# Performance work log

Measured on AMD Instinct MI355X. Metric: run time of the kernel, lower is better.

Reference implementation:

```python
import jax, jax.numpy as jnp
import numpy as np

B, T, H = 2, 2048, 1024
NH_R, HD_R = 4, 256            # RWKV6 heads / head_dim
EXP, HD_M = 2, 64
DI = EXP * H                   # mamba inner = 2048
NH_M = DI // HD_M              # 32 mamba heads
DS = 128                       # mamba d_state
CK = 4                         # causal conv kernel
FFN = 4 * H
EPS = 1e-6


def rms(x, w, eps=EPS):
    return w * x * jax.lax.rsqrt(jnp.mean(x * x, -1, keepdims=True) + eps)


def setup_inputs() -> dict:
    key = jax.random.key(0)
    ks = iter(jax.random.split(key, 32))
    def w(shape, scale=0.02):
        return jax.random.normal(next(ks), shape, jnp.float32) * scale
    return dict(
        x=w((B, T, H), 1.0),
        ln_w=jnp.ones((H,), jnp.float32),
        r_w=w((H, H)), k_w=w((H, H)), v_w=w((H, H)), g_w=w((H, H)), dw_w=w((H, H)),
        u=w((NH_R, HD_R), 0.5),
        gn_w=jnp.ones((H,), jnp.float32),
        o_w=w((H, H)),
        in_proj=w((H, 2 * DI + 2 * DS + NH_M)),
        conv_w=w((DI + 2 * DS, CK), 0.1),
        conv_b=jnp.zeros((DI + 2 * DS,), jnp.float32),
        dt_bias=w((NH_M,), 0.1),
        A_log=jnp.log(jnp.arange(1, NH_M + 1, dtype=jnp.float32)),
        D_m=w((NH_M,), 0.5),
        m_norm_w=jnp.ones((DI,), jnp.float32),
        out_proj=w((DI, H)),
        gate_w=jnp.zeros((2 * H, 1), jnp.float32),   # zero-init per module
        gate_b=jnp.zeros((1,), jnp.float32),         # logit(0.5) = 0
        ffn_ln_w=jnp.ones((H,), jnp.float32),
        ffn_w1=w((H, FFN)),
        ffn_w2=w((FFN, H)),
    )


def _rwkv6(nx, r_w, k_w, v_w, g_w, dw_w, u, gn_w, o_w):
    r = (nx @ r_w).reshape(B, T, NH_R, HD_R)
    k = (nx @ k_w).reshape(B, T, NH_R, HD_R)
    v = (nx @ v_w).reshape(B, T, NH_R, HD_R)
    g = jax.nn.silu(nx @ g_w)                                  # output gate
    wdec = jnp.exp(-jnp.exp(nx @ dw_w)).reshape(B, T, NH_R, HD_R)  # data-dep decay in (0,1)
    tm = lambda a: a.transpose(1, 0, 2, 3)                     # [T,B,h,d]

    def step(S, inp):  # S: [B,h,K,V]
        rt, kt, vt, wt = inp
        kv = kt[..., :, None] * vt[..., None, :]
        o = jnp.einsum('bhk,bhkv->bhv', rt, S + u[..., :, None] * kv)
        return wt[..., :, None] * S + kv, o

    S0 = jnp.zeros((B, NH_R, HD_R, HD_R), nx.dtype)
    _, o = jax.lax.scan(step, S0, (tm(r), tm(k), tm(v), tm(wdec)))
    o = o.transpose(1, 0, 2, 3)                                # [B,T,h,d]
    o = o * jax.lax.rsqrt(jnp.mean(o * o, -1, keepdims=True) + EPS)  # per-head RMS (group norm)
    o = o.reshape(B, T, H) * gn_w
    return (o * g) @ o_w


def _mamba2(nx, in_proj, conv_w, conv_b, dt_bias, A_log, D_m, m_norm_w, out_proj):
    zxbcdt = nx @ in_proj
    z, xBC, dt = jnp.split(zxbcdt, [DI, 2 * DI + 2 * DS], axis=-1)
    xp = jnp.pad(xBC, ((0, 0), (CK - 1, 0), (0, 0)))           # causal depthwise conv
    xBC = sum(xp[:, i:i + T, :] * conv_w[:, i] for i in range(CK)) + conv_b
    xBC = jax.nn.silu(xBC)
    xm, Bm, Cm = jnp.split(xBC, [DI, DI + DS], axis=-1)
    xm = xm.reshape(B, T, NH_M, HD_M)
    dt = jax.nn.softplus(dt + dt_bias)                          # [B,T,nh]
    A = -jnp.exp(A_log)                                         # [nh]

    def step(h, inp):  # h: [B,nh,hd,ds]
        xt, Bt, Ct, dtt = inp
        h = h * jnp.exp(dtt * A)[..., None, None] + (dtt[..., None] * xt)[..., None] * Bt[:, None, None, :]
        y = jnp.einsum('bhds,bs->bhd', h, Ct)
        return h, y

    h0 = jnp.zeros((B, NH_M, HD_M, DS), nx.dtype)
    _, y = jax.lax.scan(step, h0, (xm.transpose(1, 0, 2, 3), Bm.transpose(1, 0, 2), Cm.transpose(1, 0, 2), dt.transpose(1, 0, 2)))
    y = y.transpose(1, 0, 2, 3) + D_m[None, None, :, None] * xm
    y = y.reshape(B, T, DI)
    y = rms(y * jax.nn.silu(z), m_norm_w)                       # gated RMSNorm
    return y @ out_proj


def reference(x, ln_w, r_w, k_w, v_w, g_w, dw_w, u, gn_w, o_w,
              in_proj, conv_w, conv_b, dt_bias, A_log, D_m, m_norm_w, out_proj,
              gate_w, gate_b, ffn_ln_w, ffn_w1, ffn_w2):
    nx = rms(x, ln_w)
    o_r = _rwkv6(nx, r_w, k_w, v_w, g_w, dw_w, u, gn_w, o_w)
    o_m = _mamba2(nx, in_proj, conv_w, conv_b, dt_bias, A_log, D_m, m_norm_w, out_proj)
    gate = jax.nn.sigmoid(jnp.concatenate([o_r, o_m], -1) @ gate_w + gate_b)  # [B,T,1]
    x = x + gate * o_r + (1.0 - gate) * o_m
    x = x + jax.nn.gelu(rms(x, ffn_ln_w) @ ffn_w1, approximate=False) @ ffn_w2
    return x
```

## Files before the change

### kernel.cpp

```cpp
#include <hip/hip_runtime.h>
#include <hip/hip_bf16.h>
#include <stdint.h>

#define B_ 2
#define T_ 2048
#define H_ 1024
#define M_ 4096
#define DI 2048
#define DS 128
#define CONVD 2304
#define LD2 4480
#define EPS_ 1e-6f

typedef __bf16 bf16x8 __attribute__((ext_vector_type(8)));
typedef float f32x4 __attribute__((ext_vector_type(4)));
typedef uint32_t u32x4 __attribute__((ext_vector_type(4)));

__device__ __forceinline__ unsigned short f2bfu(float f) {
    union { float f; uint32_t u; } a; a.f = f;
    uint32_t r = a.u + 0x7FFFu + ((a.u >> 16) & 1u);
    return (unsigned short)(r >> 16);
}
__device__ __forceinline__ float bfu2f(unsigned short u) {
    union { uint32_t u; float f; } a; a.u = ((uint32_t)u) << 16; return a.f;
}
__device__ __forceinline__ float siluf(float x) { return x / (1.f + expf(-x)); }
__device__ __forceinline__ bf16x8 zero8() { bf16x8 r{}; return r; }

__global__ __launch_bounds__(256) void k_rms1024(const float* __restrict__ in, const float* __restrict__ w,
                                                 unsigned short* __restrict__ out) {
    __shared__ float red[4];
    int m = blockIdx.x, tid = threadIdx.x;
    size_t base = (size_t)m * H_ + tid * 4;
    float4 v = *(const float4*)(in + base);
    float ss = v.x * v.x + v.y * v.y + v.z * v.z + v.w * v.w;
#pragma unroll
    for (int off = 32; off; off >>= 1) ss += __shfl_xor(ss, off);
    if ((tid & 63) == 0) red[tid >> 6] = ss;
    __syncthreads();
    float scale = rsqrtf((red[0] + red[1] + red[2] + red[3]) * (1.f / 1024.f) + EPS_);
    float4 wv = *(const float4*)(w + tid * 4);
    ushort4 o;
    o.x = f2bfu(v.x * wv.x * scale); o.y = f2bfu(v.y * wv.y * scale);
    o.z = f2bfu(v.z * wv.z * scale); o.w = f2bfu(v.w * wv.w * scale);
    *(ushort4*)(out + base) = o;
}

__global__ __launch_bounds__(256) void k_transpose(const float* __restrict__ src, unsigned short* __restrict__ dst,
                                                   int K, int N, int NP) {
    __shared__ float t[32][33];
    int n0 = blockIdx.x * 32, k0 = blockIdx.y * 32;
    int tx = threadIdx.x & 31, ty = threadIdx.x >> 5;
#pragma unroll
    for (int i = ty; i < 32; i += 8) {
        int k = k0 + i, n = n0 + tx;
        t[i][tx] = (n < N) ? src[(size_t)k * N + n] : 0.f;
    }
    __syncthreads();
#pragma unroll
    for (int i = ty; i < 32; i += 8) {
        int n = n0 + i, k = k0 + tx;
        if (n < NP) dst[(size_t)n * K + k] = f2bfu(t[tx][i]);
    }
}

template <int EPI>
__global__ __launch_bounds__(256) void k_gemm(const unsigned short* __restrict__ A, const unsigned short* __restrict__ Bt,
                                              void* __restrict__ Cout, const float* __restrict__ aux,
                                              int M, int N, int K) {
    __shared__ alignas(16) unsigned short As[128 * 64];
    __shared__ alignas(16) unsigned short Bs[128 * 64];
    const int tid = threadIdx.x;
    const int m0 = blockIdx.y * 128, n0 = blockIdx.x * 128;
    const int wave = tid >> 6, lane = tid & 63;
    const int wm = (wave >> 1) * 64, wn = (wave & 1) * 64;
    const int fr = lane & 15, fg = lane >> 4;
    const int srow = tid >> 3;
    const int ske = (tid & 7) * 8;

    f32x4 acc[4][4];
#pragma unroll
    for (int m = 0; m < 4; m++)
#pragma unroll
        for (int n = 0; n < 4; n++) acc[m][n] = (f32x4)(0.f);

    const int nk = K >> 6;
    u32x4 ra[4], rb[4];
#pragma unroll
    for (int i = 0; i < 4; i++) {
        ra[i] = *(const u32x4*)(A + (size_t)(m0 + srow + 32 * i) * K + ske);
        rb[i] = *(const u32x4*)(Bt + (size_t)(n0 + srow + 32 * i) * K + ske);
    }
    for (int kt = 0; kt < nk; ++kt) {
        __syncthreads();
#pragma unroll
        for (int i = 0; i < 4; i++) {
            int lin = (tid + 256 * i) * 16;
            int sw = lin ^ (((lin >> 7) & 7) << 4);
            *(u32x4*)((char*)As + sw) = ra[i];
            *(u32x4*)((char*)Bs + sw) = rb[i];
        }
        __syncthreads();
        if (kt + 1 < nk) {
#pragma unroll
            for (int i = 0; i < 4; i++) {
                ra[i] = *(const u32x4*)(A + (size_t)(m0 + srow + 32 * i) * K + (kt + 1) * 64 + ske);
                rb[i] = *(const u32x4*)(Bt + (size_t)(n0 + srow + 32 * i) * K + (kt + 1) * 64 + ske);
            }
        }
#pragma unroll
        for (int ks = 0; ks < 2; ++ks) {
            bf16x8 af[4], bg[4];
#pragma unroll
            for (int m = 0; m < 4; m++) {
                int row = wm + m * 16 + fr;
                int lin = row * 128 + ks * 64 + fg * 16;
                af[m] = *(const bf16x8*)((const char*)As + (lin ^ ((row & 7) << 4)));
            }
#pragma unroll
            for (int n = 0; n < 4; n++) {
                int col = wn + n * 16 + fr;
                int lin = col * 128 + ks * 64 + fg * 16;
                bg[n] = *(const bf16x8*)((const char*)Bs + (lin ^ ((col & 7) << 4)));
            }
#pragma unroll
            for (int m = 0; m < 4; m++)
#pragma unroll
                for (int n = 0; n < 4; n++)
                    acc[m][n] = __builtin_amdgcn_mfma_f32_16x16x32_bf16(af[m], bg[n], acc[m][n], 0, 0, 0);
        }
    }
#pragma unroll
    for (int m = 0; m < 4; m++) {
#pragma unroll
        for (int r = 0; r < 4; r++) {
            size_t row = (size_t)(m0 + wm + m * 16 + fg * 4 + r);
#pragma unroll
            for (int n = 0; n < 4; n++) {
                size_t idx = row * N + n0 + wn + n * 16 + fr;
                float v = acc[m][n][r];
                if constexpr (EPI == 0) ((float*)Cout)[idx] = v;
                else if constexpr (EPI == 4) ((unsigned short*)Cout)[idx] = f2bfu(0.5f * v * (1.f + erff(v * 0.70710678118f)));
                else ((float*)Cout)[idx] = v + aux[idx];
            }
        }
    }
}

__global__ __launch_bounds__(256) void k_gemm_fused(const unsigned short* __restrict__ A, const unsigned short* __restrict__ Bt,
                                                    unsigned short* __restrict__ RB, unsigned short* __restrict__ KB,
                                                    unsigned short* __restrict__ VB, unsigned short* __restrict__ GB,
                                                    float* __restrict__ WF, unsigned short* __restrict__ C2B) {
    __shared__ alignas(16) unsigned short As[128 * 64];
    __shared__ alignas(16) unsigned short Bs[128 * 64];
    const int tid = threadIdx.x;
    const int m0 = blockIdx.y * 128, n0 = blockIdx.x * 128;
    const int wave = tid >> 6, lane = tid & 63;
    const int wm = (wave >> 1) * 64, wn = (wave & 1) * 64;
    const int fr = lane & 15, fg = lane >> 4;
    const int srow = tid >> 3;
    const int ske = (tid & 7) * 8;
    const int K = 1024;

    f32x4 acc[4][4];
#pragma unroll
    for (int m = 0; m < 4; m++)
#pragma unroll
        for (int n = 0; n < 4; n++) acc[m][n] = (f32x4)(0.f);

    u32x4 ra[4], rb[4];
#pragma unroll
    for (int i = 0; i < 4; i++) {
        ra[i] = *(const u32x4*)(A + (size_t)(m0 + srow + 32 * i) * K + ske);
        rb[i] = *(const u32x4*)(Bt + (size_t)(n0 + srow + 32 * i) * K + ske);
    }
    for (int kt = 0; kt < 16; ++kt) {
        __syncthreads();
#pragma unroll
        for (int i = 0; i < 4; i++) {
            int lin = (tid + 256 * i) * 16;
            int sw = lin ^ (((lin >> 7) & 7) << 4);
            *(u32x4*)((char*)As + sw) = ra[i];
            *(u32x4*)((char*)Bs + sw) = rb[i];
        }
        __syncthreads();
        if (kt + 1 < 16) {
#pragma unroll
            for (int i = 0; i < 4; i++) {
                ra[i] = *(const u32x4*)(A + (size_t)(m0 + srow + 32 * i) * K + (kt + 1) * 64 + ske);
                rb[i] = *(const u32x4*)(Bt + (size_t)(n0 + srow + 32 * i) * K + (kt + 1) * 64 + ske);
            }
        }
#pragma unroll
        for (int ks = 0; ks < 2; ++ks) {
            bf16x8 af[4], bg[4];
#pragma unroll
            for (int m = 0; m < 4; m++) {
                int row = wm + m * 16 + fr;
                int lin = row * 128 + ks * 64 + fg * 16;
                af[m] = *(const bf16x8*)((const char*)As + (lin ^ ((row & 7) << 4)));
            }
#pragma unroll
            for (int n = 0; n < 4; n++) {
                int col = wn + n * 16 + fr;
                int lin = col * 128 + ks * 64 + fg * 16;
                bg[n] = *(const bf16x8*)((const char*)Bs + (lin ^ ((col & 7) << 4)));
            }
#pragma unroll
            for (int m = 0; m < 4; m++)
#pragma unroll
                for (int n = 0; n < 4; n++)
                    acc[m][n] = __builtin_amdgcn_mfma_f32_16x16x32_bf16(af[m], bg[n], acc[m][n], 0, 0, 0);
        }
    }
    const int seg = n0 >> 10;
#pragma unroll
    for (int m = 0; m < 4; m++) {
#pragma unroll
        for (int r = 0; r < 4; r++) {
            size_t row = (size_t)(m0 + wm + m * 16 + fg * 4 + r);
#pragma unroll
            for (int n = 0; n < 4; n++) {
                int gcol = n0 + wn + n * 16 + fr;
                float v = acc[m][n][r];
                if (n0 < 5120) {
                    size_t idx = row * 1024 + (gcol & 1023);
                    if (seg == 0) RB[idx] = f2bfu(v);
                    else if (seg == 1) KB[idx] = f2bfu(v);
                    else if (seg == 2) VB[idx] = f2bfu(v);
                    else if (seg == 3) GB[idx] = f2bfu(siluf(v));
                    else WF[idx] = expf(-expf(v));
                } else {
                    C2B[row * 4480 + (gcol - 5120)] = f2bfu(v);
                }
            }
        }
    }
}

__global__ __launch_bounds__(256) void k_rwkv_prep(unsigned short* __restrict__ RB, unsigned short* __restrict__ KB,
                                                   const float* __restrict__ WF, const float* __restrict__ u,
                                                   unsigned short* __restrict__ KDt, unsigned short* __restrict__ QLb,
                                                   float* __restrict__ DDb) {
    __shared__ float red[16][257];
    __shared__ float red2[16][17];
    const int c = blockIdx.x, bh = blockIdx.y;
    const int b = bh >> 2, h = bh & 3;
    const int k = threadIdx.x;
    const size_t m0 = (size_t)b * T_ + c * 16;
    const int hk = h * 256 + k;
    const float uv = u[hk];
    float Q = 1.f;
    float kd[16];
#pragma unroll
    for (int s = 0; s < 16; s++) {
        size_t off = (m0 + s) * H_ + hk;
        float r = bfu2f(RB[off]);
        float kv = bfu2f(KB[off]);
        float w = WF[off];
        RB[off] = f2bfu(r * Q);
        Q = fmaxf(Q * w, 1e-35f);
        float kdv = kv / Q;
        kd[s] = kdv;
        KB[off] = f2bfu(kdv);
        red[s][k] = r * uv * kv;
    }
    QLb[((size_t)(b * 128 + c)) * 1024 + hk] = f2bfu(Q);
    size_t kt0 = (((size_t)(b * 128 + c)) * 1024 + hk) * 16;
#pragma unroll
    for (int s = 0; s < 16; s++) KDt[kt0 + s] = f2bfu(kd[s]);
    __syncthreads();
    {
        int s = threadIdx.x >> 4, part = threadIdx.x & 15;
        float ps = 0.f;
#pragma unroll
        for (int j = 0; j < 16; j++) ps += red[s][part * 16 + j];
        red2[s][part] = ps;
    }
    __syncthreads();
    if (threadIdx.x < 32) {
        int s = threadIdx.x & 15, half = threadIdx.x >> 4;
        float d = 0.f;
#pragma unroll
        for (int j = 0; j < 8; j++) d += red2[s][half * 8 + j];
        DDb[(((size_t)bh * 128 + c) * 2 + half) * 16 + s] = d;
    }
}

__global__ __launch_bounds__(256) void k_rwkv_carry(const unsigned short* __restrict__ KD, const unsigned short* __restrict__ VB,
                                                    const unsigned short* __restrict__ QLb, unsigned short* __restrict__ Scc) {
    __shared__ unsigned short kds[16][256];
    __shared__ float lv[16][4];
    const int vg = blockIdx.x, bh = blockIdx.y;
    const int b = bh >> 2, h = bh & 3;
    const int k = threadIdx.x;
    const int hk = h * 256 + k;
    const size_t baseM = (size_t)b * T_;
    float s0 = 0.f, s1 = 0.f, s2 = 0.f, s3 = 0.f;
    for (int c = 0; c < 128; ++c) {
        size_t m0 = baseM + c * 16;
        if ((c & 7) == 0 && c > 0) {
            int cc = c >> 3;
            size_t sb = ((size_t)(bh * 16 + cc) * 256 + vg * 4) * 256 + k;
            Scc[sb] = f2bfu(s0); Scc[sb + 256] = f2bfu(s1);
            Scc[sb + 512] = f2bfu(s2); Scc[sb + 768] = f2bfu(s3);
        }
        __syncthreads();
#pragma unroll
        for (int it = 0; it < 2; ++it) {
            int i = threadIdx.x + it * 256;
            int row = i >> 5, col8 = (i & 31) * 8;
            *(u32x4*)&kds[row][col8] = *(const u32x4*)(KD + (m0 + row) * H_ + h * 256 + col8);
        }
        if (threadIdx.x < 64) {
            int t = threadIdx.x >> 2, j = threadIdx.x & 3;
            lv[t][j] = bfu2f(VB[(m0 + t) * H_ + h * 256 + vg * 4 + j]);
        }
        __syncthreads();
        float a0 = 0.f, a1 = 0.f, a2 = 0.f, a3 = 0.f;
#pragma unroll
        for (int t = 0; t < 16; t++) {
            float kdv = bfu2f(kds[t][k]);
            a0 = fmaf(kdv, lv[t][0], a0);
            a1 = fmaf(kdv, lv[t][1], a1);
            a2 = fmaf(kdv, lv[t][2], a2);
            a3 = fmaf(kdv, lv[t][3], a3);
        }
        float ql = bfu2f(QLb[((size_t)(b * 128 + c)) * 1024 + hk]);
        s0 = (s0 + a0) * ql; s1 = (s1 + a1) * ql;
        s2 = (s2 + a2) * ql; s3 = (s3 + a3) * ql;
    }
}

__global__ __launch_bounds__(256) void k_rwkv_out(const unsigned short* __restrict__ RT, const unsigned short* __restrict__ KD,
                                                  const unsigned short* __restrict__ KDt, const unsigned short* __restrict__ VB,
                                                  const unsigned short* __restrict__ QLb, const float* __restrict__ DDb,
                                                  const unsigned short* __restrict__ Scc,
                                                  float* __restrict__ P0, float* __restrict__ P1) {
    __shared__ unsigned short Sb[64][136];
    __shared__ unsigned short VT[64][24];
    __shared__ unsigned short Ab[16][24];
    __shared__ float dls[16];
    const int tid = threadIdx.x;
    const int vt = blockIdx.x, cc = blockIdx.y;
    const int bh = blockIdx.z >> 1, kh = blockIdx.z & 1;
    const int b = bh >> 2, h = bh & 3;
    const int wave = tid >> 6, lane = tid & 63;
    const int l16 = lane & 15, lq = lane >> 4;
    const int wv0 = wave * 16;
    const int hk0 = h * 256 + kh * 128;
    const int hv = h * 256 + vt * 64;
    const int aoff = (lq < 2) ? lq * 8 : 0;
    float* __restrict__ OP = kh ? P1 : P0;
    f32x4 sreg[8];
    if (cc == 0) {
#pragma unroll
        for (int kt = 0; kt < 8; kt++) sreg[kt] = (f32x4)(0.f);
        for (int i = tid; i < 64 * 136 / 8; i += 256) ((u32x4*)Sb)[i] = (u32x4)(0u);
    } else {
        size_t sbase = ((size_t)(bh * 16 + cc) * 256 + vt * 64);
        for (int i = tid; i < 1024; i += 256) {
            int v = i >> 4, k8 = (i & 15) * 8;
            *(u32x4*)&Sb[v][k8] = *(const u32x4*)(Scc + (sbase + v) * 256 + kh * 128 + k8);
        }
#pragma unroll
        for (int kt = 0; kt < 8; kt++) {
            ushort4 w4 = *(const ushort4*)(Scc + (sbase + wv0 + l16) * 256 + kh * 128 + kt * 16 + lq * 4);
            sreg[kt][0] = bfu2f(w4.x); sreg[kt][1] = bfu2f(w4.y);
            sreg[kt][2] = bfu2f(w4.z); sreg[kt][3] = bfu2f(w4.w);
        }
    }
    __syncthreads();

    for (int fc = 0; fc < 8; ++fc) {
        const int c = cc * 8 + fc;
        const size_t m0 = (size_t)b * T_ + c * 16;
        const size_t bc = (size_t)(b * 128 + c);
        if (fc > 0) __syncthreads();
        {
            int st = tid >> 4, v4 = (tid & 15) * 4;
            ushort4 v4v = *(const ushort4*)(VB + (m0 + st) * H_ + hv + v4);
            VT[v4 + 0][st] = v4v.x; VT[v4 + 1][st] = v4v.y;
            VT[v4 + 2][st] = v4v.z; VT[v4 + 3][st] = v4v.w;
            if (tid < 16) dls[tid] = DDb[(((size_t)bh * 128 + c) * 2 + kh) * 16 + tid];
        }
        __syncthreads();
        const size_t rowA = (m0 + l16) * H_ + hk0;
        bf16x8 rtf[4];
#pragma unroll
        for (int ks = 0; ks < 4; ks++) rtf[ks] = *(const bf16x8*)(RT + rowA + ks * 32 + lq * 8);
        f32x4 Aacc = (f32x4)(0.f);
#pragma unroll
        for (int ks = 0; ks < 4; ks++) {
            bf16x8 kdf = *(const bf16x8*)(KD + rowA + ks * 32 + lq * 8);
            Aacc = __builtin_amdgcn_mfma_f32_16x16x32_bf16(rtf[ks], kdf, Aacc, 0, 0, 0);
        }
        f32x4 oacc = (f32x4)(0.f);
#pragma unroll
        for (int ks = 0; ks < 4; ks++) {
            bf16x8 sbf = *(const bf16x8*)(&Sb[wv0 + l16][ks * 32 + lq * 8]);
            oacc = __builtin_amdgcn_mfma_f32_16x16x32_bf16(rtf[ks], sbf, oacc, 0, 0, 0);
        }
#pragma unroll
        for (int r = 0; r < 4; r++) {
            int t = lq * 4 + r, s = l16;
            float av = (s < t) ? Aacc[r] : ((s == t) ? dls[t] : 0.f);
            Ab[t][s] = f2bfu(av);
        }
        bf16x8 abf_t = *(const bf16x8*)(&Ab[l16][aoff]);
        bf16x8 vtf_t = *(const bf16x8*)(&VT[wv0 + l16][aoff]);
        bf16x8 abf = (lq < 2) ? abf_t : zero8();
        bf16x8 vtf = (lq < 2) ? vtf_t : zero8();
        oacc = __builtin_amdgcn_mfma_f32_16x16x32_bf16(abf, vtf, oacc, 0, 0, 0);
#pragma unroll
        for (int r = 0; r < 4; r++)
            OP[(m0 + lq * 4 + r) * H_ + hv + wv0 + l16] = oacc[r];
#pragma unroll
        for (int kt = 0; kt < 8; kt++) {
            const unsigned short* kp = KDt + (((bc * 1024) + hk0 + kt * 16 + l16) << 4) + aoff;
            bf16x8 kdtf_t = *(const bf16x8*)kp;
            bf16x8 kdtf = (lq < 2) ? kdtf_t : zero8();
            sreg[kt] = __builtin_amdgcn_mfma_f32_16x16x32_bf16(kdtf, vtf, sreg[kt], 0, 0, 0);
            ushort4 q4 = *(const ushort4*)(QLb + bc * 1024 + hk0 + kt * 16 + lq * 4);
            sreg[kt][0] *= bfu2f(q4.x); sreg[kt][1] *= bfu2f(q4.y);
            sreg[kt][2] *= bfu2f(q4.z); sreg[kt][3] *= bfu2f(q4.w);
            ushort4 pk;
            pk.x = f2bfu(sreg[kt][0]); pk.y = f2bfu(sreg[kt][1]);
            pk.z = f2bfu(sreg[kt][2]); pk.w = f2bfu(sreg[kt][3]);
            *(ushort4*)(&Sb[wv0 + l16][kt * 16 + lq * 4]) = pk;
        }
    }
}

__global__ __launch_bounds__(256) void k_rwkv_post(const float* __restrict__ P0, const float* __restrict__ P1,
                                                   const float* __restrict__ gn_w, unsigned short* __restrict__ g_io) {
    int m = blockIdx.x, tid = threadIdx.x;
    int wave = tid >> 6, lane = tid & 63;
    size_t base = (size_t)m * H_ + wave * 256 + lane * 4;
    int col = wave * 256 + lane * 4;
    float4 a = *(const float4*)(P0 + base);
    float4 b4 = *(const float4*)(P1 + base);
    float4 v; v.x = a.x + b4.x; v.y = a.y + b4.y; v.z = a.z + b4.z; v.w = a.w + b4.w;
    float ss = v.x * v.x + v.y * v.y + v.z * v.z + v.w * v.w;
#pragma unroll
    for (int off = 32; off; off >>= 1) ss += __shfl_xor(ss, off);
    float scale = rsqrtf(ss * (1.f / 256.f) + EPS_);
    float4 gn = *(const float4*)(gn_w + col);
    ushort4 gb4 = *(const ushort4*)(g_io + base);
    ushort4 out;
    out.x = f2bfu(v.x * scale * gn.x * bfu2f(gb4.x));
    out.y = f2bfu(v.y * scale * gn.y * bfu2f(gb4.y));
    out.z = f2bfu(v.z * scale * gn.z * bfu2f(gb4.z));
    out.w = f2bfu(v.w * scale * gn.w * bfu2f(gb4.w));
    *(ushort4*)(g_io + base) = out;
}

__global__ __launch_bounds__(256) void k_conv(const unsigned short* __restrict__ C2B, const float* __restrict__ conv_w,
                                              const float* __restrict__ conv_b, unsigned short* __restrict__ XB,
                                              float* __restrict__ BCF) {
    int m = blockIdx.y;
    int c = blockIdx.x * 256 + threadIdx.x;
    int b = m >> 11, t = m & 2047;
    float acc = conv_b[c];
#pragma unroll
    for (int i = 0; i < 4; i++) {
        int tt = t - 3 + i;
        if (tt >= 0) acc = fmaf(bfu2f(C2B[((size_t)(b * T_ + tt)) * LD2 + DI + c]), conv_w[c * 4 + i], acc);
    }
    float r = siluf(acc);
    if (c < DI) XB[(size_t)m * DI + c] = f2bfu(r);
    else BCF[(size_t)m * 256 + (c - DI)] = r;
}

#define MT 32
__global__ __launch_bounds__(256, 2) void k_mamba_scan(const unsigned short* __restrict__ C2B, const unsigned short* __restrict__ XB,
                                                       const float* __restrict__ BCF,
                                                       const float* __restrict__ dt_bias, const float* __restrict__ A_log,
                                                       unsigned short* __restrict__ Y0, unsigned short* __restrict__ Y1) {
    __shared__ float lB[MT][64], lC[MT][64], lx[MT][16], lda[MT], ldt[MT];
    __shared__ float pst[MT * 272];
    const int tid = threadIdx.x;
    const int d0 = blockIdx.x * 16;
    const int sh = blockIdx.y;
    const int bh = blockIdx.z;
    const int b = bh >> 5, h = bh & 31;
    const int wave = tid >> 6, lane = tid & 63;
    const int dloc = wave * 4 + (lane >> 4);
    const int li = lane & 15;
    const size_t baseM = (size_t)b * T_;
    const float A = -expf(A_log[h]);
    const float dtb = dt_bias[h];
    unsigned short* __restrict__ YP = sh ? Y1 : Y0;
    float hS[4] = {0.f, 0.f, 0.f, 0.f};

    for (int c = 0; c < T_ / MT; ++c) {
        __syncthreads();
        int t0 = c * MT;
#pragma unroll
        for (int it = 0; it < 2; ++it) {
            int idx = (tid + it * 256) * 4;
            int tt = idx >> 6, s = idx & 63;
            const float* src = BCF + (baseM + t0 + tt) * 256 + sh * 64 + s;
            *(float4*)&lB[tt][s] = *(const float4*)(src);
            *(float4*)&lC[tt][s] = *(const float4*)(src + 128);
        }
#pragma unroll
        for (int it = 0; it < 2; ++it) {
            int idx = tid + it * 256;
            int tt = idx >> 4, i = idx & 15;
            lx[tt][i] = bfu2f(XB[(baseM + t0 + tt) * DI + h * 64 + d0 + i]);
        }
        if (tid < MT) {
            float draw = bfu2f(C2B[(baseM + t0 + tid) * LD2 + 4352 + h]) + dtb;
            float ds = draw > 20.f ? draw : log1pf(expf(draw));
            ldt[tid] = ds;
            lda[tid] = expf(A * ds);
        }
        __syncthreads();
#pragma unroll 1
        for (int tt = 0; tt < MT; ++tt) {
            float da = lda[tt];
            float dtx = ldt[tt] * lx[tt][dloc];
            float4 Bv = *(const float4*)&lB[tt][li * 4];
            float4 Cv = *(const float4*)&lC[tt][li * 4];
            hS[0] = fmaf(hS[0], da, dtx * Bv.x);
            hS[1] = fmaf(hS[1], da, dtx * Bv.y);
            hS[2] = fmaf(hS[2], da, dtx * Bv.z);
            hS[3] = fmaf(hS[3], da, dtx * Bv.w);
            float p0 = fmaf(hS[1], Cv.y, hS[0] * Cv.x);
            float p1 = fmaf(hS[3], Cv.w, hS[2] * Cv.z);
            pst[tt * 272 + dloc * 17 + li] = p0 + p1;
        }
        __syncthreads();
        {
            int tt = tid >> 3, dl = tid & 7;
            const float* row0 = &pst[tt * 272 + dl * 17];
            const float* row1 = &pst[tt * 272 + (dl + 8) * 17];
            float s0 = 0.f, s1 = 0.f;
#pragma unroll
            for (int j = 0; j < 16; j++) { s0 += row0[j]; s1 += row1[j]; }
            size_t orow = (baseM + t0 + tt) * DI + h * 64 + d0;
            YP[orow + dl] = f2bfu(s0);
            YP[orow + dl + 8] = f2bfu(s1);
        }
    }
}

__global__ __launch_bounds__(256) void k_mamba_post(unsigned short* __restrict__ y_io, const unsigned short* __restrict__ y1,
                                                    const unsigned short* __restrict__ XB,
                                                    const unsigned short* __restrict__ C2B, const float* __restrict__ D_m,
                                                    const float* __restrict__ mnw) {
    __shared__ float red[4];
    int m = blockIdx.x, tid = threadIdx.x;
    int j0 = tid * 8;
    const float Dv = D_m[j0 >> 6];
    ushort4 ya = *(const ushort4*)(y_io + (size_t)m * DI + j0);
    ushort4 yb = *(const ushort4*)(y_io + (size_t)m * DI + j0 + 4);
    ushort4 wa = *(const ushort4*)(y1 + (size_t)m * DI + j0);
    ushort4 wb = *(const ushort4*)(y1 + (size_t)m * DI + j0 + 4);
    ushort4 xa = *(const ushort4*)(XB + (size_t)m * DI + j0);
    ushort4 xb = *(const ushort4*)(XB + (size_t)m * DI + j0 + 4);
    ushort4 za = *(const ushort4*)(C2B + (size_t)m * LD2 + j0);
    ushort4 zb = *(const ushort4*)(C2B + (size_t)m * LD2 + j0 + 4);
    float yv[8] = {bfu2f(ya.x) + bfu2f(wa.x), bfu2f(ya.y) + bfu2f(wa.y), bfu2f(ya.z) + bfu2f(wa.z), bfu2f(ya.w) + bfu2f(wa.w),
                   bfu2f(yb.x) + bfu2f(wb.x), bfu2f(yb.y) + bfu2f(wb.y), bfu2f(yb.z) + bfu2f(wb.z), bfu2f(yb.w) + bfu2f(wb.w)};
    float xv[8] = {bfu2f(xa.x), bfu2f(xa.y), bfu2f(xa.z), bfu2f(xa.w), bfu2f(xb.x), bfu2f(xb.y), bfu2f(xb.z), bfu2f(xb.w)};
    float zv[8] = {bfu2f(za.x), bfu2f(za.y), bfu2f(za.z), bfu2f(za.w), bfu2f(zb.x), bfu2f(zb.y), bfu2f(zb.z), bfu2f(zb.w)};
    float val[8];
    float ss = 0.f;
#pragma unroll
    for (int i = 0; i < 8; i++) {
        float v = (yv[i] + Dv * xv[i]) * siluf(zv[i]);
        val[i] = v;
        ss += v * v;
    }
#pragma unroll
    for (int off = 32; off; off >>= 1) ss += __shfl_xor(ss, off);
    if ((tid & 63) == 0) red[tid >> 6] = ss;
    __syncthreads();
    float scale = rsqrtf((red[0] + red[1] + red[2] + red[3]) * (1.f / 2048.f) + EPS_);
    ushort4 oa, ob;
    oa.x = f2bfu(val[0] * scale * mnw[j0 + 0]); oa.y = f2bfu(val[1] * scale * mnw[j0 + 1]);
    oa.z = f2bfu(val[2] * scale * mnw[j0 + 2]); oa.w = f2bfu(val[3] * scale * mnw[j0 + 3]);
    ob.x = f2bfu(val[4] * scale * mnw[j0 + 4]); ob.y = f2bfu(val[5] * scale * mnw[j0 + 5]);
    ob.z = f2bfu(val[6] * scale * mnw[j0 + 6]); ob.w = f2bfu(val[7] * scale * mnw[j0 + 7]);
    *(ushort4*)(y_io + (size_t)m * DI + j0) = oa;
    *(ushort4*)(y_io + (size_t)m * DI + j0 + 4) = ob;
}

__global__ __launch_bounds__(256) void k_mix(const float* __restrict__ x, const float* __restrict__ o_r,
                                             const float* __restrict__ o_m, const float* __restrict__ gw,
                                             const float* __restrict__ gb, const float* __restrict__ flnw,
                                             float* __restrict__ x1, unsigned short* __restrict__ nx2) {
    __shared__ float red[4];
    int m = blockIdx.x, tid = threadIdx.x;
    size_t base = (size_t)m * H_ + tid * 4;
    float4 orv = *(const float4*)(o_r + base);
    float4 omv = *(const float4*)(o_m + base);
    float4 xv = *(const float4*)(x + base);
    float4 g1 = *(const float4*)(gw + tid * 4);
    float4 g2 = *(const float4*)(gw + 1024 + tid * 4);
    float ps = orv.x * g1.x + orv.y * g1.y + orv.z * g1.z + orv.w * g1.w
             + omv.x * g2.x + omv.y * g2.y + omv.z * g2.z + omv.w * g2.w;
#pragma unroll
    for (int off = 32; off; off >>= 1) ps += __shfl_xor(ps, off);
    if ((tid & 63) == 0) red[tid >> 6] = ps;
    __syncthreads();
    float g = 1.f / (1.f + expf(-(red[0] + red[1] + red[2] + red[3] + gb[0])));
    float4 xo;
    xo.x = xv.x + g * orv.x + (1.f - g) * omv.x;
    xo.y = xv.y + g * orv.y + (1.f - g) * omv.y;
    xo.z = xv.z + g * orv.z + (1.f - g) * omv.z;
    xo.w = xv.w + g * orv.w + (1.f - g) * omv.w;
    *(float4*)(x1 + base) = xo;
    float ss = xo.x * xo.x + xo.y * xo.y + xo.z * xo.z + xo.w * xo.w;
#pragma unroll
    for (int off = 32; off; off >>= 1) ss += __shfl_xor(ss, off);
    __syncthreads();
    if ((tid & 63) == 0) red[tid >> 6] = ss;
    __syncthreads();
    float scale = rsqrtf((red[0] + red[1] + red[2] + red[3]) * (1.f / 1024.f) + EPS_);
    float4 wv = *(const float4*)(flnw + tid * 4);
    ushort4 o;
    o.x = f2bfu(xo.x * scale * wv.x); o.y = f2bfu(xo.y * scale * wv.y);
    o.z = f2bfu(xo.z * scale * wv.z); o.w = f2bfu(xo.w * scale * wv.w);
    *(ushort4*)(nx2 + base) = o;
}

extern "C" void kernel_launch(void* const* d_in, const int* in_sizes, int n_in,
                              void* d_out, int out_size, void* d_ws, size_t ws_size,
                              hipStream_t stream) {
    const float* x = (const float*)d_in[0];
    const float* ln_w = (const float*)d_in[1];
    const float* r_w = (const float*)d_in[2];
    const float* k_w = (const float*)d_in[3];
    const float* v_w = (const float*)d_in[4];
    const float* g_w = (const float*)d_in[5];
    const float* dw_w = (const float*)d_in[6];
    const float* u = (const float*)d_in[7];
    const float* gn_w = (const float*)d_in[8];
    const float* o_w = (const float*)d_in[9];
    const float* in_proj = (const float*)d_in[10];
    const float* conv_w = (const float*)d_in[11];
    const float* conv_b = (const float*)d_in[12];
    const float* dt_bias = (const float*)d_in[13];
    const float* A_log = (const float*)d_in[14];
    const float* D_m = (const float*)d_in[15];
    const float* m_norm_w = (const float*)d_in[16];
    const float* out_proj = (const float*)d_in[17];
    const float* gate_w = (const float*)d_in[18];
    const float* gate_b = (const float*)d_in[19];
    const float* ffn_ln_w = (const float*)d_in[20];
    const float* ffn_w1 = (const float*)d_in[21];
    const float* ffn_w2 = (const float*)d_in[22];
    (void)in_sizes; (void)n_in;

    const size_t NEEDED = 192675840ull;
    if (ws_size < NEEDED) {
        hipMemsetAsync(d_out, 0, (size_t)out_size * 4, stream);
        return;
    }
    char* ws = (char*)d_ws;
    unsigned short* WT5 = (unsigned short*)(ws + 0);
    unsigned short* INPT = (unsigned short*)(ws + 10485760);
    unsigned short* QLb = (unsigned short*)(ws + 0);
    float* DDb = (float*)(ws + 524288);
    unsigned short* SCC = (unsigned short*)(ws + 1048576);
    unsigned short* F1T = (unsigned short*)(ws + 0);
    unsigned short* F2T = (unsigned short*)(ws + 10485760);
    unsigned short* OWT = (unsigned short*)(ws + 19660800);
    unsigned short* OPT = (unsigned short*)(ws + 21757952);
    unsigned short* NXB = (unsigned short*)(ws + 25952256);
    unsigned short* KDt = NXB;
    unsigned short* RB = (unsigned short*)(ws + 34340864);
    unsigned short* KB = (unsigned short*)(ws + 42729472);
    unsigned short* VB = (unsigned short*)(ws + 51118080);
    unsigned short* GB = (unsigned short*)(ws + 59506688);
    float* WF = (float*)(ws + 67895296);
    unsigned short* Y1 = (unsigned short*)(ws + 67895296);
    float* OM = (float*)(ws + 34340864);
    unsigned short* MIDB = (unsigned short*)(ws + 51118080);
    unsigned short* C2B = (unsigned short*)(ws + 84672512);
    unsigned short* XB = (unsigned short*)(ws + 121372672);
    float* BCF = (float*)(ws + 138149888);
    float* P0 = (float*)(ws + 142344192);
    float* P1 = (float*)(ws + 159121408);
    unsigned short* YB = (unsigned short*)(ws + 175898624);

    dim3 blk(256);
    k_rms1024<<<M_, blk, 0, stream>>>(x, ln_w, NXB);
    k_transpose<<<dim3(32, 32), blk, 0, stream>>>(r_w, WT5 + 0ull * 1048576, 1024, 1024, 1024);
    k_transpose<<<dim3(32, 32), blk, 0, stream>>>(k_w, WT5 + 1ull * 1048576, 1024, 1024, 1024);
    k_transpose<<<dim3(32, 32), blk, 0, stream>>>(v_w, WT5 + 2ull * 1048576, 1024, 1024, 1024);
    k_transpose<<<dim3(32, 32), blk, 0, stream>>>(g_w, WT5 + 3ull * 1048576, 1024, 1024, 1024);
    k_transpose<<<dim3(32, 32), blk, 0, stream>>>(dw_w, WT5 + 4ull * 1048576, 1024, 1024, 1024);
    k_transpose<<<dim3(140, 32), blk, 0, stream>>>(in_proj, INPT, 1024, 4384, 4480);
    k_transpose<<<dim3(32, 32), blk, 0, stream>>>(o_w, OWT, 1024, 1024, 1024);
    k_transpose<<<dim3(32, 64), blk, 0, stream>>>(out_proj, OPT, 2048, 1024, 1024);
    k_gemm_fused<<<dim3(75, 32), blk, 0, stream>>>(NXB, WT5, RB, KB, VB, GB, WF, C2B);
    k_conv<<<dim3(9, M_), blk, 0, stream>>>(C2B, conv_w, conv_b, XB, BCF);
    k_rwkv_prep<<<dim3(128, 8), blk, 0, stream>>>(RB, KB, WF, u, KDt, QLb, DDb);
    k_rwkv_carry<<<dim3(64, 8), blk, 0, stream>>>(KB, VB, QLb, SCC);
    k_rwkv_out<<<dim3(4, 16, 16), blk, 0, stream>>>(RB, KB, KDt, VB, QLb, DDb, SCC, P0, P1);
    k_rwkv_post<<<M_, blk, 0, stream>>>(P0, P1, gn_w, GB);
    k_transpose<<<dim3(128, 32), blk, 0, stream>>>(ffn_w1, F1T, 1024, 4096, 4096);
    k_transpose<<<dim3(32, 128), blk, 0, stream>>>(ffn_w2, F2T, 4096, 1024, 1024);
    k_mamba_scan<<<dim3(4, 2, 64), blk, 0, stream>>>(C2B, XB, BCF, dt_bias, A_log, YB, Y1);
    k_mamba_post<<<M_, blk, 0, stream>>>(YB, Y1, XB, C2B, D_m, m_norm_w);
    k_gemm<0><<<dim3(8, 32), blk, 0, stream>>>(GB, OWT, P1, nullptr, 4096, 1024, 1024);
    k_gemm<0><<<dim3(8, 32), blk, 0, stream>>>(YB, OPT, OM, nullptr, 4096, 1024, 2048);
    k_mix<<<M_, blk, 0, stream>>>(x, P1, OM, gate_w, gate_b, ffn_ln_w, P0, NXB);
    k_gemm<4><<<dim3(32, 32), blk, 0, stream>>>(NXB, F1T, MIDB, nullptr, 4096, 4096, 1024);
    k_gemm<5><<<dim3(8, 32), blk, 0, stream>>>(MIDB, F2T, (float*)d_out, P0, 4096, 1024, 4096);
}
```

Before: 1.044 ms.

## Split mamba scan state dimension four ways for more parallel blocks

The Mamba selective scan now splits the 128-wide state dimension into four 32-wide slices instead of two 64-wide slices. This doubles the block count, halves per-thread state, shortens the time chunk to 16 and raises occupancy. The post kernel sums four bf16 partial outputs instead of two, which adds memory traffic and extra bf16 rounding. The scan is also moved ahead of the FFN weight transposes so two extra partial buffers can reuse workspace regions that are free at that point.

```diff
diff --git a/kernel.cpp b/kernel.cpp
--- a/kernel.cpp
+++ b/kernel.cpp
@@ -472,45 +472,44 @@
     else BCF[(size_t)m * 256 + (c - DI)] = r;
 }
 
-#define MT 32
-__global__ __launch_bounds__(256, 2) void k_mamba_scan(const unsigned short* __restrict__ C2B, const unsigned short* __restrict__ XB,
+#define MT2 16
+__global__ __launch_bounds__(256, 4) void k_mamba_scan(const unsigned short* __restrict__ C2B, const unsigned short* __restrict__ XB,
                                                        const float* __restrict__ BCF,
                                                        const float* __restrict__ dt_bias, const float* __restrict__ A_log,
-                                                       unsigned short* __restrict__ Y0, unsigned short* __restrict__ Y1) {
-    __shared__ float lB[MT][64], lC[MT][64], lx[MT][16], lda[MT], ldt[MT];
-    __shared__ float pst[MT * 272];
+                                                       unsigned short* __restrict__ Y0, unsigned short* __restrict__ Y1,
+                                                       unsigned short* __restrict__ Y2, unsigned short* __restrict__ Y3) {
+    __shared__ float lB[MT2][32], lC[MT2][32], lx[MT2][16], lda[MT2], ldt[MT2];
+    __shared__ float pst[MT2 * 272];
     const int tid = threadIdx.x;
     const int d0 = blockIdx.x * 16;
-    const int sh = blockIdx.y;
+    const int sq = blockIdx.y;
     const int bh = blockIdx.z;
     const int b = bh >> 5, h = bh & 31;
-    const int wave = tid >> 6, lane = tid & 63;
-    const int dloc = wave * 4 + (lane >> 4);
-    const int li = lane & 15;
+    const int dloc = tid >> 4;
+    const int li = tid & 15;
     const size_t baseM = (size_t)b * T_;
     const float A = -expf(A_log[h]);
     const float dtb = dt_bias[h];
-    unsigned short* __restrict__ YP = sh ? Y1 : Y0;
-    float hS[4] = {0.f, 0.f, 0.f, 0.f};
-
-    for (int c = 0; c < T_ / MT; ++c) {
-        __syncthreads();
-        int t0 = c * MT;
-#pragma unroll
-        for (int it = 0; it < 2; ++it) {
-            int idx = (tid + it * 256) * 4;
-            int tt = idx >> 6, s = idx & 63;
-            const float* src = BCF + (baseM + t0 + tt) * 256 + sh * 64 + s;
-            *(float4*)&lB[tt][s] = *(const float4*)(src);
-            *(float4*)&lC[tt][s] = *(const float4*)(src + 128);
-        }
-#pragma unroll
-        for (int it = 0; it < 2; ++it) {
-            int idx = tid + it * 256;
-            int tt = idx >> 4, i = idx & 15;
+    unsigned short* __restrict__ YP = (sq == 0) ? Y0 : (sq == 1) ? Y1 : (sq == 2) ? Y2 : Y3;
+    float h0 = 0.f, h1 = 0.f;
+    const int sbuf = tid >> 7;
+    const int sj = (tid & 127) * 4;
+
+    for (int c = 0; c < T_ / MT2; ++c) {
+        __syncthreads();
+        int t0 = c * MT2;
+        {
+            int tt = sj >> 5, s = sj & 31;
+            const float* src = BCF + (baseM + t0 + tt) * 256 + (sbuf ? 128 : 0) + sq * 32 + s;
+            float4 v4 = *(const float4*)src;
+            if (sbuf == 0) *(float4*)&lB[tt][s] = v4;
+            else *(float4*)&lC[tt][s] = v4;
+        }
+        {
+            int tt = tid >> 4, i = tid & 15;
             lx[tt][i] = bfu2f(XB[(baseM + t0 + tt) * DI + h * 64 + d0 + i]);
         }
-        if (tid < MT) {
+        if (tid < MT2) {
             float draw = bfu2f(C2B[(baseM + t0 + tid) * LD2 + 4352 + h]) + dtb;
             float ds = draw > 20.f ? draw : log1pf(expf(draw));
             ldt[tid] = ds;
@@ -518,35 +517,29 @@
         }
         __syncthreads();
 #pragma unroll 1
-        for (int tt = 0; tt < MT; ++tt) {
+        for (int tt = 0; tt < MT2; ++tt) {
             float da = lda[tt];
             float dtx = ldt[tt] * lx[tt][dloc];
-            float4 Bv = *(const float4*)&lB[tt][li * 4];
-            float4 Cv = *(const float4*)&lC[tt][li * 4];
-            hS[0] = fmaf(hS[0], da, dtx * Bv.x);
-            hS[1] = fmaf(hS[1], da, dtx * Bv.y);
-            hS[2] = fmaf(hS[2], da, dtx * Bv.z);
-            hS[3] = fmaf(hS[3], da, dtx * Bv.w);
-            float p0 = fmaf(hS[1], Cv.y, hS[0] * Cv.x);
-            float p1 = fmaf(hS[3], Cv.w, hS[2] * Cv.z);
-            pst[tt * 272 + dloc * 17 + li] = p0 + p1;
+            float2 Bv = *(const float2*)&lB[tt][li * 2];
+            float2 Cv = *(const float2*)&lC[tt][li * 2];
+            h0 = fmaf(h0, da, dtx * Bv.x);
+            h1 = fmaf(h1, da, dtx * Bv.y);
+            pst[tt * 272 + dloc * 17 + li] = fmaf(h0, Cv.x, h1 * Cv.y);
         }
         __syncthreads();
         {
-            int tt = tid >> 3, dl = tid & 7;
-            const float* row0 = &pst[tt * 272 + dl * 17];
-            const float* row1 = &pst[tt * 272 + (dl + 8) * 17];
-            float s0 = 0.f, s1 = 0.f;
-#pragma unroll
-            for (int j = 0; j < 16; j++) { s0 += row0[j]; s1 += row1[j]; }
-            size_t orow = (baseM + t0 + tt) * DI + h * 64 + d0;
-            YP[orow + dl] = f2bfu(s0);
-            YP[orow + dl + 8] = f2bfu(s1);
+            int tt = tid >> 4, d = tid & 15;
+            const float* row = &pst[tt * 272 + d * 17];
+            float s = 0.f;
+#pragma unroll
+            for (int j = 0; j < 16; j++) s += row[j];
+            YP[(baseM + t0 + tt) * DI + h * 64 + d0 + d] = f2bfu(s);
         }
     }
 }
 
 __global__ __launch_bounds__(256) void k_mamba_post(unsigned short* __restrict__ y_io, const unsigned short* __restrict__ y1,
+                                                    const unsigned short* __restrict__ y2, const unsigned short* __restrict__ y3,
                                                     const unsigned short* __restrict__ XB,
                                                     const unsigned short* __restrict__ C2B, const float* __restrict__ D_m,
                                                     const float* __restrict__ mnw) {
@@ -556,14 +549,24 @@
     const float Dv = D_m[j0 >> 6];
     ushort4 ya = *(const ushort4*)(y_io + (size_t)m * DI + j0);
     ushort4 yb = *(const ushort4*)(y_io + (size_t)m * DI + j0 + 4);
-    ushort4 wa = *(const ushort4*)(y1 + (size_t)m * DI + j0);
-    ushort4 wb = *(const ushort4*)(y1 + (size_t)m * DI + j0 + 4);
+    ushort4 pa = *(const ushort4*)(y1 + (size_t)m * DI + j0);
+    ushort4 pb = *(const ushort4*)(y1 + (size_t)m * DI + j0 + 4);
+    ushort4 qa = *(const ushort4*)(y2 + (size_t)m * DI + j0);
+    ushort4 qb = *(const ushort4*)(y2 + (size_t)m * DI + j0 + 4);
+    ushort4 ra = *(const ushort4*)(y3 + (size_t)m * DI + j0);
+    ushort4 rb = *(const ushort4*)(y3 + (size_t)m * DI + j0 + 4);
     ushort4 xa = *(const ushort4*)(XB + (size_t)m * DI + j0);
     ushort4 xb = *(const ushort4*)(XB + (size_t)m * DI + j0 + 4);
     ushort4 za = *(const ushort4*)(C2B + (size_t)m * LD2 + j0);
     ushort4 zb = *(const ushort4*)(C2B + (size_t)m * LD2 + j0 + 4);
-    float yv[8] = {bfu2f(ya.x) + bfu2f(wa.x), bfu2f(ya.y) + bfu2f(wa.y), bfu2f(ya.z) + bfu2f(wa.z), bfu2f(ya.w) + bfu2f(wa.w),
-                   bfu2f(yb.x) + bfu2f(wb.x), bfu2f(yb.y) + bfu2f(wb.y), bfu2f(yb.z) + bfu2f(wb.z), bfu2f(yb.w) + bfu2f(wb.w)};
+    float yv[8] = {bfu2f(ya.x) + bfu2f(pa.x) + bfu2f(qa.x) + bfu2f(ra.x),
+                   bfu2f(ya.y) + bfu2f(pa.y) + bfu2f(qa.y) + bfu2f(ra.y),
+                   bfu2f(ya.z) + bfu2f(pa.z) + bfu2f(qa.z) + bfu2f(ra.z),
+                   bfu2f(ya.w) + bfu2f(pa.w) + bfu2f(qa.w) + bfu2f(ra.w),
+                   bfu2f(yb.x) + bfu2f(pb.x) + bfu2f(qb.x) + bfu2f(rb.x),
+                   bfu2f(yb.y) + bfu2f(pb.y) + bfu2f(qb.y) + bfu2f(rb.y),
+                   bfu2f(yb.z) + bfu2f(pb.z) + bfu2f(qb.z) + bfu2f(rb.z),
+                   bfu2f(yb.w) + bfu2f(pb.w) + bfu2f(qb.w) + bfu2f(rb.w)};
     float xv[8] = {bfu2f(xa.x), bfu2f(xa.y), bfu2f(xa.z), bfu2f(xa.w), bfu2f(xb.x), bfu2f(xb.y), bfu2f(xb.z), bfu2f(xb.w)};
     float zv[8] = {bfu2f(za.x), bfu2f(za.y), bfu2f(za.z), bfu2f(za.w), bfu2f(zb.x), bfu2f(zb.y), bfu2f(zb.z), bfu2f(zb.w)};
     float val[8];
@@ -666,6 +669,7 @@
     unsigned short* QLb = (unsigned short*)(ws + 0);
     float* DDb = (float*)(ws + 524288);
     unsigned short* SCC = (unsigned short*)(ws + 1048576);
+    unsigned short* Y2 = (unsigned short*)(ws + 1048576);
     unsigned short* F1T = (unsigned short*)(ws + 0);
     unsigned short* F2T = (unsigned short*)(ws + 10485760);
     unsigned short* OWT = (unsigned short*)(ws + 19660800);
@@ -674,6 +678,7 @@
     unsigned short* KDt = NXB;
     unsigned short* RB = (unsigned short*)(ws + 34340864);
     unsigned short* KB = (unsigned short*)(ws + 42729472);
+    unsigned short* Y3 = (unsigned short*)(ws + 34340864);
     unsigned short* VB = (unsigned short*)(ws + 51118080);
     unsigned short* GB = (unsigned short*)(ws + 59506688);
     float* WF = (float*)(ws + 67895296);
@@ -703,10 +708,10 @@
     k_rwkv_carry<<<dim3(64, 8), blk, 0, stream>>>(KB, VB, QLb, SCC);
     k_rwkv_out<<<dim3(4, 16, 16), blk, 0, stream>>>(RB, KB, KDt, VB, QLb, DDb, SCC, P0, P1);
     k_rwkv_post<<<M_, blk, 0, stream>>>(P0, P1, gn_w, GB);
+    k_mamba_scan<<<dim3(4, 4, 64), blk, 0, stream>>>(C2B, XB, BCF, dt_bias, A_log, YB, Y1, Y2, Y3);
+    k_mamba_post<<<M_, blk, 0, stream>>>(YB, Y1, Y2, Y3, XB, C2B, D_m, m_norm_w);
     k_transpose<<<dim3(128, 32), blk, 0, stream>>>(ffn_w1, F1T, 1024, 4096, 4096);
     k_transpose<<<dim3(32, 128), blk, 0, stream>>>(ffn_w2, F2T, 4096, 1024, 1024);
-    k_mamba_scan<<<dim3(4, 2, 64), blk, 0, stream>>>(C2B, XB, BCF, dt_bias, A_log, YB, Y1);
-    k_mamba_post<<<M_, blk, 0, stream>>>(YB, Y1, XB, C2B, D_m, m_norm_w);
     k_gemm<0><<<dim3(8, 32), blk, 0, stream>>>(GB, OWT, P1, nullptr, 4096, 1024, 1024);
     k_gemm<0><<<dim3(8, 32), blk, 0, stream>>>(YB, OPT, OM, nullptr, 4096, 1024, 2048);
     k_mix<<<M_, blk, 0, stream>>>(x, P1, OM, gate_w, gate_b, ffn_ln_w, P0, NXB);
```

Measured after the change: 1.143 ms. 9.5% more time.
